# Optimization experiments

Hardware: AMD Instinct MI355X
Metric: run time of the kernel (lower is better)

## Reference

```python
import jax, jax.numpy as jnp
import numpy as np


def setup_inputs() -> dict:
    key = jax.random.key(0)
    k1, k2, k3, k4 = jax.random.split(key, 4)
    B, Lq, Lk, D = 16, 2048, 2048, 128
    return {
        "query": jax.random.normal(k1, (B, Lq, D), dtype=jnp.float32),
        "key": jax.random.normal(k2, (B, Lk, D), dtype=jnp.float32),
        "value": jax.random.normal(k3, (B, Lk, D), dtype=jnp.float32),
        "valid_len": jax.random.randint(k4, (B,), 1, Lk + 1, dtype=jnp.int32),
    }


def reference(query, key, value, valid_len):
    # score[b, i, j] = <query[b,i,:], key[b,j,:]> / sqrt(D)
    D = query.shape[-1]
    score = jnp.einsum("bqd,bkd->bqk", query, key) / jnp.sqrt(jnp.asarray(D, query.dtype))
    # masked softmax over key positions: j >= valid_len[b] -> masked
    Lk = key.shape[1]
    mask = jnp.arange(Lk)[None, None, :] < valid_len[:, None, None]  # [B,1,Lk]
    score = jnp.where(mask, score, jnp.asarray(-1e6, score.dtype))
    attn = jax.nn.softmax(score, axis=-1)
    # dropout p=0.0 (eval) -> identity
    return jnp.einsum("bqk,bkd->bqd", attn, value)
```

## Files before the change

kernel.cpp:

```cpp
#include <hip/hip_runtime.h>
#include <stdint.h>

typedef __attribute__((ext_vector_type(8)))  short short8;
typedef __attribute__((ext_vector_type(16))) float f32x16;
typedef __attribute__((ext_vector_type(4)))  float f32x4;
typedef __attribute__((ext_vector_type(2)))  float f32x2;

union U8 { short8 s; unsigned u[4]; };

__device__ __forceinline__ unsigned short f2bf(float x){
  unsigned u = __float_as_uint(x);
  u += 0x7fffu + ((u >> 16) & 1u);
  return (unsigned short)(u >> 16);
}
__device__ __forceinline__ unsigned pk2(float lo, float hi){
  return (unsigned)f2bf(lo) | ((unsigned)f2bf(hi) << 16);
}
__device__ __forceinline__ void swap32(unsigned &a, unsigned &b){
  asm("v_permlane32_swap_b32 %0, %1" : "+v"(a), "+v"(b));
}

#define MFMA32(a,b,c) __builtin_amdgcn_mfma_f32_32x32x16_bf16((a),(b),(c),0,0,0)

__global__ void prep_kv(const float* __restrict__ K, const float* __restrict__ V,
                        const int* __restrict__ VL,
                        char* __restrict__ Kws, char* __restrict__ Vws, int Lk)
{
  const int b = blockIdx.y, t = blockIdx.x, tid = threadIdx.x;
  if (t * 64 >= VL[b]) return;
  const int kv0 = t * 64;
  const size_t tbase = ((size_t)b * (Lk >> 6) + t) << 14;
  const float* Kg = K + ((size_t)b * Lk + kv0) * 128;
  const float* Vg = V + ((size_t)b * Lk + kv0) * 128;
  {
    const int key = tid >> 2;
    const int c0  = (tid & 3) * 4;
    const float* kp = Kg + key * 128 + c0 * 8;
    f32x4 ka[8];
#pragma unroll
    for (int i = 0; i < 8; ++i) ka[i] = *(const f32x4*)(kp + i * 4);
    char* kb = Kws + tbase + key * 256;
#pragma unroll
    for (int i = 0; i < 4; ++i) {
      U8 u;
      u.u[0] = pk2(ka[2*i].x,   ka[2*i].y);
      u.u[1] = pk2(ka[2*i].z,   ka[2*i].w);
      u.u[2] = pk2(ka[2*i+1].x, ka[2*i+1].y);
      u.u[3] = pk2(ka[2*i+1].z, ka[2*i+1].w);
      *(short8*)(kb + (((c0 + i) ^ (key & 7)) * 16)) = u.s;
    }
  }
  {
    const int kvp = (tid >> 3) * 2;
    const int d0  = (tid & 7) * 16;
    const float* vp = Vg + kvp * 128 + d0;
    f32x4 va[4], vb[4];
#pragma unroll
    for (int i = 0; i < 4; ++i) {
      va[i] = *(const f32x4*)(vp + i * 4);
      vb[i] = *(const f32x4*)(vp + 128 + i * 4);
    }
    char* vbse = Vws + tbase;
#pragma unroll
    for (int j = 0; j < 16; ++j) {
      const int d  = d0 + j;
      const unsigned wv = pk2(va[j >> 2][j & 3], vb[j >> 2][j & 3]);
      const int bp = (kvp >> 3) ^ ((d >> 4) & 7) ^ (d & 7);
      *(unsigned*)(vbse + d * 128 + bp * 16 + (kvp & 7) * 2) = wv;
    }
  }
}

__device__ __forceinline__ void issue_tile2(char* sm, int g, int buf,
                                            const char* Kt, const char* Vt,
                                            int gt, int wl, int lane)
{
  const size_t goff = ((size_t)gt << 14) + (size_t)(wl * 4096 + lane * 16);
  const char* gk = Kt + goff;
  const char* gv = Vt + goff;
  char* lk = sm + (g << 15) + (buf << 14) + wl * 4096;
  char* lv = lk + 65536;
#pragma unroll
  for (int i = 0; i < 4; ++i) {
    __builtin_amdgcn_global_load_lds((const __attribute__((address_space(1))) void*)(gk + i * 1024),
                                     (__attribute__((address_space(3))) void*)(lk + i * 1024), 16, 0, 0);
    __builtin_amdgcn_global_load_lds((const __attribute__((address_space(1))) void*)(gv + i * 1024),
                                     (__attribute__((address_space(3))) void*)(lv + i * 1024), 16, 0, 0);
  }
}

__launch_bounds__(512, 1)
__global__ void attn_ws2(const float* __restrict__ Q, const char* __restrict__ Kws,
                         const char* __restrict__ Vws, const int* __restrict__ VL,
                         float* __restrict__ Out, int Lq, int Lk)
{
  __shared__ __align__(16) char sm[132096];
  const int tid  = threadIdx.x;
  const int lane = tid & 63;
  const int w    = tid >> 6;
  const int wl   = w & 3;
  const int g    = w >> 2;
  const int lq   = lane & 31;
  const int hi   = lane >> 5;

  int qt, b;
  if (gridDim.x == 256 && gridDim.y == 1) {
    const int bid = blockIdx.x;
    b  = (bid & 7) | (((bid >> 3) & 1) << 3);
    qt = bid >> 4;
  } else { qt = blockIdx.x; b = blockIdx.y; }

  const int vlb   = VL[b];
  const int ntall = (vlb + 63) >> 6;
  const int ntA   = (ntall + 1) >> 1;
  const int myn   = g ? (ntall - ntA) : ntA;
  const int t0    = g ? ntA : 0;
  const float SCL2 = 0.08838834764831845f * 1.4426950408889634f;

  const char* Ktiles = Kws + (((size_t)b * (Lk >> 6)) << 14);
  const char* Vtiles = Vws + (((size_t)b * (Lk >> 6)) << 14);

  if (myn > 0) issue_tile2(sm, g, 0, Ktiles, Vtiles, t0, wl, lane);

  const int qrow  = qt * 128 + wl * 32 + lq;
  const float* Qg = Q + ((size_t)b * Lq + qrow) * 128;

  short8 qf[8];
#pragma unroll
  for (int s8 = 0; s8 < 8; ++s8) {
    f32x4 a = *(const f32x4*)(Qg + s8 * 16 + hi * 8);
    f32x4 c = *(const f32x4*)(Qg + s8 * 16 + hi * 8 + 4);
    U8 u;
    u.u[0] = pk2(a.x, a.y); u.u[1] = pk2(a.z, a.w);
    u.u[2] = pk2(c.x, c.y); u.u[3] = pk2(c.z, c.w);
    qf[s8] = u.s;
  }

  f32x16 accO[4];
#pragma unroll
  for (int i = 0; i < 4; ++i)
#pragma unroll
    for (int r = 0; r < 16; ++r) accO[i][r] = 0.0f;

  float mrun = -1e30f, lsum = 0.0f;

  for (int t = 0; t < ntA; ++t) {
    __syncthreads();
    if (t + 1 < myn) issue_tile2(sm, g, (t + 1) & 1, Ktiles, Vtiles, t0 + t + 1, wl, lane);

    if (t < myn) {
      const int kbase = (g << 15) + ((t & 1) << 14);
      const int vbase = 65536 + (g << 15) + ((t & 1) << 14);

      f32x16 s0, s1;
#pragma unroll
      for (int r = 0; r < 16; ++r) { s0[r] = 0.0f; s1[r] = 0.0f; }
#pragma unroll
      for (int s8 = 0; s8 < 8; ++s8) {
        const int blk = 2 * s8 + hi;
        short8 k0 = *(const short8*)(sm + kbase + lq * 256        + ((blk ^ (lq & 7)) * 16));
        short8 k1 = *(const short8*)(sm + kbase + (32 + lq) * 256 + ((blk ^ (lq & 7)) * 16));
        s0 = MFMA32(k0, qf[s8], s0);
        s1 = MFMA32(k1, qf[s8], s1);
      }

      const int gt = t0 + t;
      if (gt == ntall - 1 && (vlb & 63)) {
        const int kb = gt * 64 + 4 * hi;
#pragma unroll
        for (int r = 0; r < 16; ++r) {
          const int key = kb + (r & 3) + 8 * (r >> 2);
          if (key >= vlb)      s0[r] = -1e30f;
          if (key + 32 >= vlb) s1[r] = -1e30f;
        }
      }

      float tmax = -1e30f;
#pragma unroll
      for (int r = 0; r < 16; ++r) { tmax = fmaxf(tmax, s0[r]); tmax = fmaxf(tmax, s1[r]); }
      tmax = fmaxf(tmax, __shfl_xor(tmax, 32, 64));
      const float mnew = fmaxf(mrun, tmax);
      const float mk   = mnew * SCL2;
      float tsum = 0.0f;
#pragma unroll
      for (int r = 0; r < 16; ++r) {
        s0[r] = __builtin_amdgcn_exp2f(s0[r] * SCL2 - mk); tsum += s0[r];
        s1[r] = __builtin_amdgcn_exp2f(s1[r] * SCL2 - mk); tsum += s1[r];
      }
      tsum += __shfl_xor(tsum, 32, 64);
      if (__any(mnew > mrun)) {
        const float corr = __builtin_amdgcn_exp2f((mrun - mnew) * SCL2);
        lsum = lsum * corr + tsum;
#pragma unroll
        for (int i = 0; i < 4; ++i)
#pragma unroll
          for (int r = 0; r < 16; ++r) accO[i][r] *= corr;
      } else {
        lsum += tsum;
      }
      mrun = mnew;

      U8 pf[4];
      {
        unsigned wt[8]; unsigned a, bx;
#pragma unroll
        for (int j = 0; j < 8; ++j) wt[j] = pk2(s0[2*j], s0[2*j+1]);
        a = wt[0]; bx = wt[2]; swap32(a, bx); pf[0].u[0] = a; pf[0].u[2] = bx;
        a = wt[1]; bx = wt[3]; swap32(a, bx); pf[0].u[1] = a; pf[0].u[3] = bx;
        a = wt[4]; bx = wt[6]; swap32(a, bx); pf[1].u[0] = a; pf[1].u[2] = bx;
        a = wt[5]; bx = wt[7]; swap32(a, bx); pf[1].u[1] = a; pf[1].u[3] = bx;
#pragma unroll
        for (int j = 0; j < 8; ++j) wt[j] = pk2(s1[2*j], s1[2*j+1]);
        a = wt[0]; bx = wt[2]; swap32(a, bx); pf[2].u[0] = a; pf[2].u[2] = bx;
        a = wt[1]; bx = wt[3]; swap32(a, bx); pf[2].u[1] = a; pf[2].u[3] = bx;
        a = wt[4]; bx = wt[6]; swap32(a, bx); pf[3].u[0] = a; pf[3].u[2] = bx;
        a = wt[5]; bx = wt[7]; swap32(a, bx); pf[3].u[1] = a; pf[3].u[3] = bx;
      }

#pragma unroll
      for (int s = 0; s < 4; ++s) {
#pragma unroll
        for (int dt = 0; dt < 4; ++dt) {
          const int d  = dt * 32 + lq;
          const int bp = (2 * s + hi) ^ ((d >> 4) & 7) ^ (d & 7);
          short8 vf = *(const short8*)(sm + vbase + d * 128 + bp * 16);
          accO[dt] = MFMA32(vf, pf[s].s, accO[dt]);
        }
      }
    }
  }

  __syncthreads();
  if (g) {
    char* pr = sm + 65536 + wl * 16384;
#pragma unroll
    for (int dt = 0; dt < 4; ++dt)
#pragma unroll
      for (int r4 = 0; r4 < 4; ++r4) {
        f32x4 o;
        o.x = accO[dt][r4*4+0]; o.y = accO[dt][r4*4+1];
        o.z = accO[dt][r4*4+2]; o.w = accO[dt][r4*4+3];
        *(f32x4*)(pr + (dt * 4 + r4) * 1024 + lane * 16) = o;
      }
    if (!hi) {
      *(float*)(sm + 131072 + wl * 256 + lq * 8)     = mrun;
      *(float*)(sm + 131072 + wl * 256 + lq * 8 + 4) = lsum;
    }
  }
  __syncthreads();
  if (!g) {
    const float m1 = *(const float*)(sm + 131072 + wl * 256 + lq * 8);
    const float l1 = *(const float*)(sm + 131072 + wl * 256 + lq * 8 + 4);
    const float m  = fmaxf(mrun, m1);
    const float a0 = __builtin_amdgcn_exp2f((mrun - m) * SCL2);
    const float a1 = __builtin_amdgcn_exp2f((m1   - m) * SCL2);
    const float lf = lsum * a0 + l1 * a1;
    const char* pr = sm + 65536 + wl * 16384;
#pragma unroll
    for (int dt = 0; dt < 4; ++dt)
#pragma unroll
      for (int r4 = 0; r4 < 4; ++r4) {
        f32x4 o1 = *(const f32x4*)(pr + (dt * 4 + r4) * 1024 + lane * 16);
        accO[dt][r4*4+0] = accO[dt][r4*4+0] * a0 + o1.x * a1;
        accO[dt][r4*4+1] = accO[dt][r4*4+1] * a0 + o1.y * a1;
        accO[dt][r4*4+2] = accO[dt][r4*4+2] * a0 + o1.z * a1;
        accO[dt][r4*4+3] = accO[dt][r4*4+3] * a0 + o1.w * a1;
      }

    const float inv = 1.0f / lf;
    char* eb = sm + wl * 16384;
#pragma unroll
    for (int dt = 0; dt < 4; ++dt) {
#pragma unroll
      for (int r = 0; r < 16; r += 2) {
        const int d = dt * 32 + (r & 3) + 8 * (r >> 2) + 4 * hi;
        f32x2 o2; o2.x = accO[dt][r] * inv; o2.y = accO[dt][r+1] * inv;
        *(f32x2*)(eb + lq * 512 + (((d >> 2) ^ (lq & 7)) * 16) + (d & 3) * 4) = o2;
      }
    }
    float* Og = Out + ((size_t)b * Lq + qt * 128 + wl * 32) * 128;
#pragma unroll
    for (int pass = 0; pass < 16; ++pass) {
      const int q = pass * 2 + hi;
      f32x4 o4 = *(const f32x4*)(eb + q * 512 + ((lq ^ (q & 7)) * 16));
      *(f32x4*)(Og + q * 128 + lq * 4) = o4;
    }
  }
}

__device__ __forceinline__ void stage_tile(char* sm, int buf, const float* __restrict__ Kg,
                                           const float* __restrict__ Vg, int kv0, int tid)
{
  {
    const int key = tid >> 2;
    const int c0  = (tid & 3) * 4;
    const float* kp = Kg + (kv0 + key) * 128 + c0 * 8;
    f32x4 ka[8];
#pragma unroll
    for (int i = 0; i < 8; ++i) ka[i] = *(const f32x4*)(kp + i * 4);
    char* kb = sm + buf * 16384 + key * 256;
#pragma unroll
    for (int i = 0; i < 4; ++i) {
      U8 u;
      u.u[0] = pk2(ka[2*i].x,   ka[2*i].y);
      u.u[1] = pk2(ka[2*i].z,   ka[2*i].w);
      u.u[2] = pk2(ka[2*i+1].x, ka[2*i+1].y);
      u.u[3] = pk2(ka[2*i+1].z, ka[2*i+1].w);
      *(short8*)(kb + (((c0 + i) ^ (key & 7)) * 16)) = u.s;
    }
  }
  {
    const int kvp = (tid >> 3) * 2;
    const int d0  = (tid & 7) * 16;
    const float* vp = Vg + (kv0 + kvp) * 128 + d0;
    f32x4 va[4], vb[4];
#pragma unroll
    for (int i = 0; i < 4; ++i) {
      va[i] = *(const f32x4*)(vp + i * 4);
      vb[i] = *(const f32x4*)(vp + 128 + i * 4);
    }
    char* vbse = sm + 32768 + buf * 16384;
#pragma unroll
    for (int j = 0; j < 16; ++j) {
      const int d  = d0 + j;
      const unsigned wv = pk2(va[j >> 2][j & 3], vb[j >> 2][j & 3]);
      const int bp = (kvp >> 3) ^ ((d >> 4) & 7) ^ (d & 7);
      *(unsigned*)(vbse + d * 128 + bp * 16 + (kvp & 7) * 2) = wv;
    }
  }
}

__launch_bounds__(256, 1)
__global__ void attn_fused(const float* __restrict__ Q, const float* __restrict__ K,
                           const float* __restrict__ V, const int* __restrict__ VL,
                           float* __restrict__ Out, int Lq, int Lk)
{
  __shared__ __align__(16) char sm[65536];
  const int tid  = threadIdx.x;
  const int lane = tid & 63;
  const int w    = tid >> 6;
  const int lq   = lane & 31;
  const int hi   = lane >> 5;
  const int b    = blockIdx.y;
  const int vlb  = VL[b];
  const int nt   = (vlb + 63) >> 6;
  const float SCL2 = 0.08838834764831845f * 1.4426950408889634f;

  const float* Kg = K + (size_t)b * Lk * 128;
  const float* Vg = V + (size_t)b * Lk * 128;
  const int qrow  = blockIdx.x * 128 + w * 32 + lq;
  const float* Qg = Q + ((size_t)b * Lq + qrow) * 128;

  short8 qf[8];
#pragma unroll
  for (int s8 = 0; s8 < 8; ++s8) {
    f32x4 a = *(const f32x4*)(Qg + s8 * 16 + hi * 8);
    f32x4 c = *(const f32x4*)(Qg + s8 * 16 + hi * 8 + 4);
    U8 u;
    u.u[0] = pk2(a.x, a.y); u.u[1] = pk2(a.z, a.w);
    u.u[2] = pk2(c.x, c.y); u.u[3] = pk2(c.z, c.w);
    qf[s8] = u.s;
  }

  f32x16 accO[4];
#pragma unroll
  for (int i = 0; i < 4; ++i)
#pragma unroll
    for (int r = 0; r < 16; ++r) accO[i][r] = 0.0f;

  float mrun = -1e30f, lsum = 0.0f;
  stage_tile(sm, 0, Kg, Vg, 0, tid);

  for (int t = 0; t < nt; ++t) {
    __syncthreads();
    const int kbase = (t & 1) * 16384;
    const int vbase = 32768 + (t & 1) * 16384;

    f32x16 s0, s1;
#pragma unroll
    for (int r = 0; r < 16; ++r) { s0[r] = 0.0f; s1[r] = 0.0f; }
#pragma unroll
    for (int s8 = 0; s8 < 8; ++s8) {
      const int blk = 2 * s8 + hi;
      short8 k0 = *(const short8*)(sm + kbase + lq * 256        + ((blk ^ (lq & 7)) * 16));
      short8 k1 = *(const short8*)(sm + kbase + (32 + lq) * 256 + ((blk ^ (lq & 7)) * 16));
      s0 = MFMA32(k0, qf[s8], s0);
      s1 = MFMA32(k1, qf[s8], s1);
    }

    if (t == nt - 1 && (vlb & 63)) {
      const int kb = t * 64 + 4 * hi;
#pragma unroll
      for (int r = 0; r < 16; ++r) {
        const int key = kb + (r & 3) + 8 * (r >> 2);
        if (key >= vlb)      s0[r] = -1e30f;
        if (key + 32 >= vlb) s1[r] = -1e30f;
      }
    }

    float tmax = -1e30f;
#pragma unroll
    for (int r = 0; r < 16; ++r) { tmax = fmaxf(tmax, s0[r]); tmax = fmaxf(tmax, s1[r]); }
    tmax = fmaxf(tmax, __shfl_xor(tmax, 32, 64));
    const float mnew = fmaxf(mrun, tmax);
    const float mk   = mnew * SCL2;
    float tsum = 0.0f;
#pragma unroll
    for (int r = 0; r < 16; ++r) {
      s0[r] = __builtin_amdgcn_exp2f(s0[r] * SCL2 - mk); tsum += s0[r];
      s1[r] = __builtin_amdgcn_exp2f(s1[r] * SCL2 - mk); tsum += s1[r];
    }
    tsum += __shfl_xor(tsum, 32, 64);
    if (__any(mnew > mrun)) {
      const float corr = __builtin_amdgcn_exp2f((mrun - mnew) * SCL2);
      lsum = lsum * corr + tsum;
#pragma unroll
      for (int i = 0; i < 4; ++i)
#pragma unroll
        for (int r = 0; r < 16; ++r) accO[i][r] *= corr;
    } else {
      lsum += tsum;
    }
    mrun = mnew;

    if (t + 1 < nt) stage_tile(sm, (t + 1) & 1, Kg, Vg, (t + 1) * 64, tid);

    U8 pf[4];
    {
      unsigned wt[8]; unsigned a, bx;
#pragma unroll
      for (int j = 0; j < 8; ++j) wt[j] = pk2(s0[2*j], s0[2*j+1]);
      a = wt[0]; bx = wt[2]; swap32(a, bx); pf[0].u[0] = a; pf[0].u[2] = bx;
      a = wt[1]; bx = wt[3]; swap32(a, bx); pf[0].u[1] = a; pf[0].u[3] = bx;
      a = wt[4]; bx = wt[6]; swap32(a, bx); pf[1].u[0] = a; pf[1].u[2] = bx;
      a = wt[5]; bx = wt[7]; swap32(a, bx); pf[1].u[1] = a; pf[1].u[3] = bx;
#pragma unroll
      for (int j = 0; j < 8; ++j) wt[j] = pk2(s1[2*j], s1[2*j+1]);
      a = wt[0]; bx = wt[2]; swap32(a, bx); pf[2].u[0] = a; pf[2].u[2] = bx;
      a = wt[1]; bx = wt[3]; swap32(a, bx); pf[2].u[1] = a; pf[2].u[3] = bx;
      a = wt[4]; bx = wt[6]; swap32(a, bx); pf[3].u[0] = a; pf[3].u[2] = bx;
      a = wt[5]; bx = wt[7]; swap32(a, bx); pf[3].u[1] = a; pf[3].u[3] = bx;
    }

#pragma unroll
    for (int s = 0; s < 4; ++s) {
#pragma unroll
      for (int dt = 0; dt < 4; ++dt) {
        const int d  = dt * 32 + lq;
        const int bp = (2 * s + hi) ^ ((d >> 4) & 7) ^ (d & 7);
        short8 vf = *(const short8*)(sm + vbase + d * 128 + bp * 16);
        accO[dt] = MFMA32(vf, pf[s].s, accO[dt]);
      }
    }
  }

  __syncthreads();
  const float inv = 1.0f / lsum;
  char* eb = sm + w * 16384;
#pragma unroll
  for (int dt = 0; dt < 4; ++dt) {
#pragma unroll
    for (int r = 0; r < 16; r += 2) {
      const int d = dt * 32 + (r & 3) + 8 * (r >> 2) + 4 * hi;
      f32x2 o2; o2.x = accO[dt][r] * inv; o2.y = accO[dt][r+1] * inv;
      *(f32x2*)(eb + lq * 512 + (((d >> 2) ^ (lq & 7)) * 16) + (d & 3) * 4) = o2;
    }
  }
  float* Og = Out + ((size_t)b * Lq + blockIdx.x * 128 + w * 32) * 128;
#pragma unroll
  for (int pass = 0; pass < 16; ++pass) {
    const int q = pass * 2 + hi;
    f32x4 o4 = *(const f32x4*)(eb + q * 512 + ((lq ^ (q & 7)) * 16));
    *(f32x4*)(Og + q * 128 + lq * 4) = o4;
  }
}

extern "C" void kernel_launch(void* const* d_in, const int* in_sizes, int n_in,
                              void* d_out, int out_size, void* d_ws, size_t ws_size,
                              hipStream_t stream)
{
  (void)n_in; (void)out_size;
  const float* Q  = (const float*)d_in[0];
  const float* K  = (const float*)d_in[1];
  const float* V  = (const float*)d_in[2];
  const int*   VL = (const int*)d_in[3];
  float* Out = (float*)d_out;
  const int B  = in_sizes[3];
  const int Lq = in_sizes[0] / (B * 128);
  const int Lk = in_sizes[1] / (B * 128);

  const size_t kbytes = (size_t)B * Lk * 256;
  const size_t need   = kbytes * 2;
  if (ws_size >= need && (Lk & 63) == 0 && (Lq & 127) == 0) {
    char* Kws = (char*)d_ws;
    char* Vws = Kws + kbytes;
    dim3 pg(Lk / 64, B);
    prep_kv<<<pg, 256, 0, stream>>>(K, V, VL, Kws, Vws, Lk);
    if (Lq == 2048 && B == 16) {
      attn_ws2<<<256, 512, 0, stream>>>(Q, Kws, Vws, VL, Out, Lq, Lk);
    } else {
      dim3 g(Lq / 128, B);
      attn_ws2<<<g, 512, 0, stream>>>(Q, Kws, Vws, VL, Out, Lq, Lk);
    }
  } else {
    dim3 g(Lq / 128, B);
    attn_fused<<<g, 256, 0, stream>>>(Q, K, V, VL, Out, Lq, Lk);
  }
}
```

Measured before the change: 58.12 us.

## Split KV sequence across four wave groups with 32-key tiles and tree merge

Doubles the block to 1024 threads so four wave groups each process interleaved 32-key tiles instead of two groups on 64-key halves, and adds a two-level tree merge of the partial softmax states. The prep kernel's K/V workspace layout is changed to 32-key half-tiles with a new V swizzle to match. The aim is more waves per CU to hide latency and better balance across groups when valid lengths are short. In exchange each tile does half the MFMA work per sync, adds extra barriers in the merge, and raises register pressure at 1024 threads.

```diff
diff --git a/kernel.cpp b/kernel.cpp
--- a/kernel.cpp
+++ b/kernel.cpp
@@ -39,7 +39,7 @@
     f32x4 ka[8];
 #pragma unroll
     for (int i = 0; i < 8; ++i) ka[i] = *(const f32x4*)(kp + i * 4);
-    char* kb = Kws + tbase + key * 256;
+    char* kb = Kws + tbase + ((key >> 5) * 8192) + (key & 31) * 256;
 #pragma unroll
     for (int i = 0; i < 4; ++i) {
       U8 u;
@@ -60,28 +60,30 @@
       va[i] = *(const f32x4*)(vp + i * 4);
       vb[i] = *(const f32x4*)(vp + 128 + i * 4);
     }
-    char* vbse = Vws + tbase;
+    char* vbse = Vws + tbase + ((kvp >> 5) * 8192);
+    const int kw = kvp & 31;
+    const int b8 = kw >> 3;
 #pragma unroll
     for (int j = 0; j < 16; ++j) {
       const int d  = d0 + j;
       const unsigned wv = pk2(va[j >> 2][j & 3], vb[j >> 2][j & 3]);
-      const int bp = (kvp >> 3) ^ ((d >> 4) & 7) ^ (d & 7);
-      *(unsigned*)(vbse + d * 128 + bp * 16 + (kvp & 7) * 2) = wv;
-    }
-  }
-}
-
-__device__ __forceinline__ void issue_tile2(char* sm, int g, int buf,
+      *(unsigned*)(vbse + d * 64 + ((b8 ^ ((d >> 1) & 3)) * 16) + (kw & 7) * 2) = wv;
+    }
+  }
+}
+
+__device__ __forceinline__ void issue_tile4(char* sm, int g, int buf,
                                             const char* Kt, const char* Vt,
-                                            int gt, int wl, int lane)
+                                            int tau, int wl, int lane)
 {
-  const size_t goff = ((size_t)gt << 14) + (size_t)(wl * 4096 + lane * 16);
+  const size_t goff = ((size_t)(tau >> 1) << 14) + ((tau & 1) << 13)
+                    + (size_t)(wl * 2048 + lane * 16);
   const char* gk = Kt + goff;
   const char* gv = Vt + goff;
-  char* lk = sm + (g << 15) + (buf << 14) + wl * 4096;
+  char* lk = sm + g * 16384 + (buf << 13) + wl * 2048;
   char* lv = lk + 65536;
 #pragma unroll
-  for (int i = 0; i < 4; ++i) {
+  for (int i = 0; i < 2; ++i) {
     __builtin_amdgcn_global_load_lds((const __attribute__((address_space(1))) void*)(gk + i * 1024),
                                      (__attribute__((address_space(3))) void*)(lk + i * 1024), 16, 0, 0);
     __builtin_amdgcn_global_load_lds((const __attribute__((address_space(1))) void*)(gv + i * 1024),
@@ -89,12 +91,12 @@
   }
 }
 
-__launch_bounds__(512, 1)
-__global__ void attn_ws2(const float* __restrict__ Q, const char* __restrict__ Kws,
+__launch_bounds__(1024, 4)
+__global__ void attn_ws4(const float* __restrict__ Q, const char* __restrict__ Kws,
                          const char* __restrict__ Vws, const int* __restrict__ VL,
                          float* __restrict__ Out, int Lq, int Lk)
 {
-  __shared__ __align__(16) char sm[132096];
+  __shared__ __align__(16) char sm[133120];
   const int tid  = threadIdx.x;
   const int lane = tid & 63;
   const int w    = tid >> 6;
@@ -110,17 +112,15 @@
     qt = bid >> 4;
   } else { qt = blockIdx.x; b = blockIdx.y; }
 
-  const int vlb   = VL[b];
-  const int ntall = (vlb + 63) >> 6;
-  const int ntA   = (ntall + 1) >> 1;
-  const int myn   = g ? (ntall - ntA) : ntA;
-  const int t0    = g ? ntA : 0;
+  const int vlb    = VL[b];
+  const int ntall  = (vlb + 31) >> 5;
+  const int nsteps = (ntall + 3) >> 2;
   const float SCL2 = 0.08838834764831845f * 1.4426950408889634f;
 
   const char* Ktiles = Kws + (((size_t)b * (Lk >> 6)) << 14);
   const char* Vtiles = Vws + (((size_t)b * (Lk >> 6)) << 14);
 
-  if (myn > 0) issue_tile2(sm, g, 0, Ktiles, Vtiles, t0, wl, lane);
+  if (g < ntall) issue_tile4(sm, g, 0, Ktiles, Vtiles, g, wl, lane);
 
   const int qrow  = qt * 128 + wl * 32 + lq;
   const float* Qg = Q + ((size_t)b * Lq + qrow) * 128;
@@ -144,40 +144,38 @@
 
   float mrun = -1e30f, lsum = 0.0f;
 
-  for (int t = 0; t < ntA; ++t) {
+  for (int t = 0; t < nsteps; ++t) {
     __syncthreads();
-    if (t + 1 < myn) issue_tile2(sm, g, (t + 1) & 1, Ktiles, Vtiles, t0 + t + 1, wl, lane);
-
-    if (t < myn) {
-      const int kbase = (g << 15) + ((t & 1) << 14);
-      const int vbase = 65536 + (g << 15) + ((t & 1) << 14);
-
-      f32x16 s0, s1;
-#pragma unroll
-      for (int r = 0; r < 16; ++r) { s0[r] = 0.0f; s1[r] = 0.0f; }
+    const int tn = (t + 1) * 4 + g;
+    if (tn < ntall) issue_tile4(sm, g, (t + 1) & 1, Ktiles, Vtiles, tn, wl, lane);
+
+    const int tau = t * 4 + g;
+    if (tau < ntall) {
+      const int kbase = g * 16384 + ((t & 1) << 13);
+      const int vbase = 65536 + kbase;
+
+      f32x16 s0;
+#pragma unroll
+      for (int r = 0; r < 16; ++r) s0[r] = 0.0f;
 #pragma unroll
       for (int s8 = 0; s8 < 8; ++s8) {
         const int blk = 2 * s8 + hi;
-        short8 k0 = *(const short8*)(sm + kbase + lq * 256        + ((blk ^ (lq & 7)) * 16));
-        short8 k1 = *(const short8*)(sm + kbase + (32 + lq) * 256 + ((blk ^ (lq & 7)) * 16));
+        short8 k0 = *(const short8*)(sm + kbase + lq * 256 + ((blk ^ (lq & 7)) * 16));
         s0 = MFMA32(k0, qf[s8], s0);
-        s1 = MFMA32(k1, qf[s8], s1);
-      }
-
-      const int gt = t0 + t;
-      if (gt == ntall - 1 && (vlb & 63)) {
-        const int kb = gt * 64 + 4 * hi;
+      }
+
+      if (tau == ntall - 1 && (vlb & 31)) {
+        const int kb = tau * 32 + 4 * hi;
 #pragma unroll
         for (int r = 0; r < 16; ++r) {
           const int key = kb + (r & 3) + 8 * (r >> 2);
-          if (key >= vlb)      s0[r] = -1e30f;
-          if (key + 32 >= vlb) s1[r] = -1e30f;
+          if (key >= vlb) s0[r] = -1e30f;
         }
       }
 
       float tmax = -1e30f;
 #pragma unroll
-      for (int r = 0; r < 16; ++r) { tmax = fmaxf(tmax, s0[r]); tmax = fmaxf(tmax, s1[r]); }
+      for (int r = 0; r < 16; ++r) tmax = fmaxf(tmax, s0[r]);
       tmax = fmaxf(tmax, __shfl_xor(tmax, 32, 64));
       const float mnew = fmaxf(mrun, tmax);
       const float mk   = mnew * SCL2;
@@ -185,7 +183,6 @@
 #pragma unroll
       for (int r = 0; r < 16; ++r) {
         s0[r] = __builtin_amdgcn_exp2f(s0[r] * SCL2 - mk); tsum += s0[r];
-        s1[r] = __builtin_amdgcn_exp2f(s1[r] * SCL2 - mk); tsum += s1[r];
       }
       tsum += __shfl_xor(tsum, 32, 64);
       if (__any(mnew > mrun)) {
@@ -200,39 +197,33 @@
       }
       mrun = mnew;
 
-      U8 pf[4];
+      U8 pf0, pf1;
       {
         unsigned wt[8]; unsigned a, bx;
 #pragma unroll
         for (int j = 0; j < 8; ++j) wt[j] = pk2(s0[2*j], s0[2*j+1]);
-        a = wt[0]; bx = wt[2]; swap32(a, bx); pf[0].u[0] = a; pf[0].u[2] = bx;
-        a = wt[1]; bx = wt[3]; swap32(a, bx); pf[0].u[1] = a; pf[0].u[3] = bx;
-        a = wt[4]; bx = wt[6]; swap32(a, bx); pf[1].u[0] = a; pf[1].u[2] = bx;
-        a = wt[5]; bx = wt[7]; swap32(a, bx); pf[1].u[1] = a; pf[1].u[3] = bx;
-#pragma unroll
-        for (int j = 0; j < 8; ++j) wt[j] = pk2(s1[2*j], s1[2*j+1]);
-        a = wt[0]; bx = wt[2]; swap32(a, bx); pf[2].u[0] = a; pf[2].u[2] = bx;
-        a = wt[1]; bx = wt[3]; swap32(a, bx); pf[2].u[1] = a; pf[2].u[3] = bx;
-        a = wt[4]; bx = wt[6]; swap32(a, bx); pf[3].u[0] = a; pf[3].u[2] = bx;
-        a = wt[5]; bx = wt[7]; swap32(a, bx); pf[3].u[1] = a; pf[3].u[3] = bx;
-      }
-
-#pragma unroll
-      for (int s = 0; s < 4; ++s) {
+        a = wt[0]; bx = wt[2]; swap32(a, bx); pf0.u[0] = a; pf0.u[2] = bx;
+        a = wt[1]; bx = wt[3]; swap32(a, bx); pf0.u[1] = a; pf0.u[3] = bx;
+        a = wt[4]; bx = wt[6]; swap32(a, bx); pf1.u[0] = a; pf1.u[2] = bx;
+        a = wt[5]; bx = wt[7]; swap32(a, bx); pf1.u[1] = a; pf1.u[3] = bx;
+      }
+
+#pragma unroll
+      for (int s = 0; s < 2; ++s) {
 #pragma unroll
         for (int dt = 0; dt < 4; ++dt) {
-          const int d  = dt * 32 + lq;
-          const int bp = (2 * s + hi) ^ ((d >> 4) & 7) ^ (d & 7);
-          short8 vf = *(const short8*)(sm + vbase + d * 128 + bp * 16);
-          accO[dt] = MFMA32(vf, pf[s].s, accO[dt]);
+          const int d    = dt * 32 + lq;
+          const int blk4 = (2 * s + hi) ^ ((d >> 1) & 3);
+          short8 vf = *(const short8*)(sm + vbase + d * 64 + blk4 * 16);
+          accO[dt] = MFMA32(vf, s ? pf1.s : pf0.s, accO[dt]);
         }
       }
     }
   }
 
   __syncthreads();
-  if (g) {
-    char* pr = sm + 65536 + wl * 16384;
+  if (g >= 2) {
+    char* pr = sm + (g - 2) * 65536 + wl * 16384;
 #pragma unroll
     for (int dt = 0; dt < 4; ++dt)
 #pragma unroll
@@ -243,19 +234,57 @@
         *(f32x4*)(pr + (dt * 4 + r4) * 1024 + lane * 16) = o;
       }
     if (!hi) {
+      *(float*)(sm + 131072 + (g - 2) * 1024 + wl * 256 + lq * 8)     = mrun;
+      *(float*)(sm + 131072 + (g - 2) * 1024 + wl * 256 + lq * 8 + 4) = lsum;
+    }
+  }
+  __syncthreads();
+  if (g < 2) {
+    const float m1 = *(const float*)(sm + 131072 + g * 1024 + wl * 256 + lq * 8);
+    const float l1 = *(const float*)(sm + 131072 + g * 1024 + wl * 256 + lq * 8 + 4);
+    const float m  = fmaxf(mrun, m1);
+    const float a0 = __builtin_amdgcn_exp2f((mrun - m) * SCL2);
+    const float a1 = __builtin_amdgcn_exp2f((m1   - m) * SCL2);
+    lsum = lsum * a0 + l1 * a1;
+    const char* pr = sm + g * 65536 + wl * 16384;
+#pragma unroll
+    for (int dt = 0; dt < 4; ++dt)
+#pragma unroll
+      for (int r4 = 0; r4 < 4; ++r4) {
+        f32x4 o1 = *(const f32x4*)(pr + (dt * 4 + r4) * 1024 + lane * 16);
+        accO[dt][r4*4+0] = accO[dt][r4*4+0] * a0 + o1.x * a1;
+        accO[dt][r4*4+1] = accO[dt][r4*4+1] * a0 + o1.y * a1;
+        accO[dt][r4*4+2] = accO[dt][r4*4+2] * a0 + o1.z * a1;
+        accO[dt][r4*4+3] = accO[dt][r4*4+3] * a0 + o1.w * a1;
+      }
+    mrun = m;
+  }
+  __syncthreads();
+  if (g == 1) {
+    char* pr = sm + wl * 16384;
+#pragma unroll
+    for (int dt = 0; dt < 4; ++dt)
+#pragma unroll
+      for (int r4 = 0; r4 < 4; ++r4) {
+        f32x4 o;
+        o.x = accO[dt][r4*4+0]; o.y = accO[dt][r4*4+1];
+        o.z = accO[dt][r4*4+2]; o.w = accO[dt][r4*4+3];
+        *(f32x4*)(pr + (dt * 4 + r4) * 1024 + lane * 16) = o;
+      }
+    if (!hi) {
       *(float*)(sm + 131072 + wl * 256 + lq * 8)     = mrun;
       *(float*)(sm + 131072 + wl * 256 + lq * 8 + 4) = lsum;
     }
   }
   __syncthreads();
-  if (!g) {
+  if (g == 0) {
     const float m1 = *(const float*)(sm + 131072 + wl * 256 + lq * 8);
     const float l1 = *(const float*)(sm + 131072 + wl * 256 + lq * 8 + 4);
     const float m  = fmaxf(mrun, m1);
     const float a0 = __builtin_amdgcn_exp2f((mrun - m) * SCL2);
     const float a1 = __builtin_amdgcn_exp2f((m1   - m) * SCL2);
     const float lf = lsum * a0 + l1 * a1;
-    const char* pr = sm + 65536 + wl * 16384;
+    const char* pr = sm + wl * 16384;
 #pragma unroll
     for (int dt = 0; dt < 4; ++dt)
 #pragma unroll
@@ -497,10 +526,10 @@
     dim3 pg(Lk / 64, B);
     prep_kv<<<pg, 256, 0, stream>>>(K, V, VL, Kws, Vws, Lk);
     if (Lq == 2048 && B == 16) {
-      attn_ws2<<<256, 512, 0, stream>>>(Q, Kws, Vws, VL, Out, Lq, Lk);
+      attn_ws4<<<256, 1024, 0, stream>>>(Q, Kws, Vws, VL, Out, Lq, Lk);
     } else {
       dim3 g(Lq / 128, B);
-      attn_ws2<<<g, 512, 0, stream>>>(Q, Kws, Vws, VL, Out, Lq, Lk);
+      attn_ws4<<<g, 1024, 0, stream>>>(Q, Kws, Vws, VL, Out, Lq, Lk);
     }
   } else {
     dim3 g(Lq / 128, B);
```

After: 86.34 us. 48.6% more time.
